# Optimization experiments

Measured on AMD Instinct MI355X. Metric: run time of the kernel, lower is better.

Reference implementation:

```python
import jax, jax.numpy as jnp
import numpy as np

B, L, H = 16, 32, 768
E, R, T = 200000, 512, 2000000
NUM_STEPS = 2
EPS = 1e-6


def setup_inputs() -> dict:
    key = jax.random.key(0)
    ks = jax.random.split(key, 16)
    s = 1.0 / np.sqrt(H)
    return {
        'heads': jax.random.uniform(ks[0], (B, E), jnp.float32),
        'q_word_h': jax.random.normal(ks[1], (B, L, H), jnp.float32),
        'attention_mask': jnp.ones((B, L), jnp.float32),
        'subj': jax.random.randint(ks[2], (T,), 0, E),
        'rel': jax.random.randint(ks[3], (T,), 0, R),
        'obj': jax.random.randint(ks[4], (T,), 0, E),
        'key_w': jax.random.normal(ks[5], (H, H), jnp.float32) * s,
        'key_b': jnp.zeros((H,), jnp.float32),
        'rel_w': jax.random.normal(ks[6], (H, R), jnp.float32) * s,
        'rel_b': jnp.zeros((R,), jnp.float32),
        'hop_w': jax.random.normal(ks[7], (H, 1), jnp.float32) * s,
        'hop_b': jnp.zeros((1,), jnp.float32),
        'hw_w': jax.random.normal(ks[8], (H, H), jnp.float32) * s,
        'hw_b': jnp.zeros((H,), jnp.float32),
    }


def _follow(e, r, subj, rel, obj, num_ent):
    # x[b,t] = e[b, subj[t]] * r[b, rel[t]]  (== Msubj@e.T * Mrel@r.T)
    x = e[:, subj] * r[:, rel]                      # [B, T]
    # scatter-add over object entities (== Mobj.T @ x)
    return jnp.zeros((e.shape[0], num_ent), e.dtype).at[:, obj].add(x)


def reference(heads, q_word_h, attention_mask, subj, rel, obj,
              key_w, key_b, rel_w, rel_b, hop_w, hop_b, hw_w, hw_b):
    mask = attention_mask[:, None, :]               # [B,1,L]
    last_e = heads
    q_hop = q_word_h
    prev_ctx = None                                  # q_word_h_dist_ctx[-1]
    ent_probs, ctx_h_list = [], []
    for t in range(NUM_STEPS):
        h_key = q_hop @ key_w + key_b                # [B,L,H]
        # torch: (h_key @ q_word_h^T)^T -> logits[b,i,j] = q_word_h[b,i].h_key[b,j]
        q_logits = jnp.einsum('bih,bjh->bij', q_word_h, h_key)
        q_dist = jax.nn.softmax(q_logits, axis=2) * mask
        q_dist = q_dist / (jnp.sum(q_dist, axis=2, keepdims=True) + EPS)
        hop_ctx = jnp.einsum('bij,bjh->bih', q_dist, q_hop)
        if t == 0:
            q_hop = q_word_h + hop_ctx
            prev_ctx = hop_ctx
        else:
            z = jax.nn.sigmoid(prev_ctx @ hw_w + hw_b)
            q_hop = q_word_h + hop_ctx + z * prev_ctx
            prev_ctx = hop_ctx + z * prev_ctx
        q_word_att = jax.nn.softmax(jnp.sum(q_dist, axis=1, keepdims=True), axis=2) * mask
        q_word_att = q_word_att / (jnp.sum(q_word_att, axis=2, keepdims=True) + EPS)  # [B,1,L]
        ctx_h = jnp.einsum('blh,bl->bh', q_hop, q_word_att[:, 0, :])
        ctx_h_list.append(ctx_h)
        rel_dist = jax.nn.sigmoid(ctx_h @ rel_w + rel_b)   # [B,R]
        new_e = _follow(last_e, rel_dist, subj, rel, obj, heads.shape[1])
        # clamp-by-division with detached scale
        z_norm = jax.lax.stop_gradient(jnp.where(new_e > 1.0, new_e, 1.0))
        last_e = new_e / z_norm
        ent_probs.append(last_e)
    hop_res = jnp.stack(ent_probs, axis=1)           # [B,S,E]
    ctx_hist = jnp.stack(ctx_h_list, axis=1)         # [B,S,H]
    hop_logit = ctx_hist @ hop_w + hop_b             # [B,S,1]
    hop_attn = jax.nn.softmax(hop_logit, axis=1)     # softmax over hops
    e_score = jnp.sum(hop_res * hop_attn, axis=1)    # [B,E]
    return e_score
```

## Files before the change

### kernel.cpp

```cpp
#include <hip/hip_runtime.h>
#include <hip/hip_bf16.h>
#include <math.h>

#define NB 16
#define NL 32
#define NH 768
#define NE 200000
#define NR 512
#define NT 2000000
#define FEPS 1e-6f

#define EB_BLOCKS ((NE + 255) / 256)

typedef float f32x4 __attribute__((ext_vector_type(4)));

__global__ __launch_bounds__(256) void k_transpose_zero(const float* __restrict__ heads,
                                                        float* __restrict__ headsT,
                                                        float* __restrict__ e0T,
                                                        float* __restrict__ e1T) {
  __shared__ float tile[256][17];
  int e0 = blockIdx.x * 256;
  int tid = threadIdx.x;
  if (e0 + tid < NE) {
#pragma unroll
    for (int b = 0; b < NB; ++b)
      tile[tid][b] = heads[(size_t)b * NE + e0 + tid];
  }
  {
    f32x4 z = {0.f, 0.f, 0.f, 0.f};
#pragma unroll
    for (int j = 0; j < 4; ++j) {
      int idx4 = j * 256 + tid;
      size_t base = (size_t)e0 * NB + idx4 * 4;
      if (base < (size_t)NE * NB) {
        *(f32x4*)(e0T + base) = z;
        *(f32x4*)(e1T + base) = z;
      }
    }
  }
  __syncthreads();
#pragma unroll
  for (int j = 0; j < 16; ++j) {
    int idx = j * 256 + tid;
    int i = idx >> 4, b = idx & 15;
    if (e0 + i < NE) headsT[(size_t)(e0 + i) * NB + b] = tile[i][b];
  }
}

__global__ __launch_bounds__(256) void k_rowmm2(const float* __restrict__ X0,
                                                const float* __restrict__ W0,
                                                const float* __restrict__ b0,
                                                float* __restrict__ Y0, int act0,
                                                const float* __restrict__ X1,
                                                const float* __restrict__ W1,
                                                const float* __restrict__ b1,
                                                float* __restrict__ Y1, int act1,
                                                int nblk0) {
  const float* X; const float* W; const float* bias; float* Y; int act, row0;
  int blk = blockIdx.x;
  if (blk < nblk0) { X = X0; W = W0; bias = b0; Y = Y0; act = act0; row0 = blk * 2; }
  else            { X = X1; W = W1; bias = b1; Y = Y1; act = act1; row0 = (blk - nblk0) * 2; }

  __shared__ float xs[2][NH];
  int tid = threadIdx.x;
  for (int r = 0; r < 2; ++r)
    for (int k = tid; k < NH; k += 256)
      xs[r][k] = X[(size_t)(row0 + r) * NH + k];
  __syncthreads();

  float acc[2][3] = {};
  for (int k = 0; k < NH; ++k) {
    float w0 = W[(size_t)k * NH + tid];
    float w1 = W[(size_t)k * NH + tid + 256];
    float w2 = W[(size_t)k * NH + tid + 512];
#pragma unroll
    for (int r = 0; r < 2; ++r) {
      float x = xs[r][k];
      acc[r][0] = fmaf(x, w0, acc[r][0]);
      acc[r][1] = fmaf(x, w1, acc[r][1]);
      acc[r][2] = fmaf(x, w2, acc[r][2]);
    }
  }
  float bb0 = bias[tid], bb1 = bias[tid + 256], bb2 = bias[tid + 512];
#pragma unroll
  for (int r = 0; r < 2; ++r) {
    size_t base = (size_t)(row0 + r) * NH;
    float y0 = acc[r][0] + bb0, y1 = acc[r][1] + bb1, y2 = acc[r][2] + bb2;
    if (act == 1) {
      y0 = 1.f / (1.f + expf(-y0));
      y1 = 1.f / (1.f + expf(-y1));
      y2 = 1.f / (1.f + expf(-y2));
    }
    Y[base + tid] = y0;
    Y[base + tid + 256] = y1;
    Y[base + tid + 512] = y2;
  }
}

template <int STEP>
__global__ __launch_bounds__(1024) void k_attn_update(const float* __restrict__ qwh,
                                                      const float* __restrict__ hkey,
                                                      const float* __restrict__ mask,
                                                      const float* __restrict__ qhop_old,
                                                      const float* __restrict__ zbuf,
                                                      const float* __restrict__ pc_old,
                                                      float* __restrict__ qhop_new,
                                                      float* __restrict__ pc_new,
                                                      float* __restrict__ ctx_h,
                                                      const float* __restrict__ rel_w,
                                                      const float* __restrict__ rel_b,
                                                      float* __restrict__ relT) {
  int b = blockIdx.x;
  int tid = threadIdx.x;
  __shared__ float qs_full[NL * NH];
  __shared__ float hks[32 * 129];
  __shared__ float qd[32 * 33];
  __shared__ float ctx_s[NH];
  __shared__ float as[NL];

#pragma unroll
  for (int it = 0; it < 6; ++it) {
    int idx4 = it * 1024 + tid;
    f32x4 v = *(const f32x4*)(qwh + (size_t)b * NL * NH + idx4 * 4);
    *(f32x4*)(qs_full + idx4 * 4) = v;
  }
  __syncthreads();

  int i = tid >> 5, j = tid & 31;
  float acc = 0.f;
  for (int k0 = 0; k0 < NH; k0 += 128) {
    {
      int jj = tid >> 5;
      int kk4 = tid & 31;
      f32x4 hv = *(const f32x4*)(hkey + ((size_t)b * NL + jj) * NH + k0 + kk4 * 4);
      int base = jj * 129 + kk4 * 4;
      hks[base] = hv.x; hks[base + 1] = hv.y; hks[base + 2] = hv.z; hks[base + 3] = hv.w;
    }
    __syncthreads();
#pragma unroll 8
    for (int kk = 0; kk < 128; ++kk)
      acc = fmaf(qs_full[i * NH + k0 + kk], hks[j * 129 + kk], acc);
    __syncthreads();
  }

  float m = acc;
  for (int s = 16; s; s >>= 1) m = fmaxf(m, __shfl_xor(m, s, 32));
  float ex = expf(acc - m);
  float sum = ex;
  for (int s = 16; s; s >>= 1) sum += __shfl_xor(sum, s, 32);
  float p = ex / sum;
  p *= mask[b * NL + j];
  float s2 = p;
  for (int s = 16; s; s >>= 1) s2 += __shfl_xor(s2, s, 32);
  p = p / (s2 + FEPS);
  qd[i * 33 + j] = p;
  __syncthreads();

  if (tid < 32) {
    int jj = tid;
    float c = 0.f;
    for (int ii = 0; ii < 32; ++ii) c += qd[ii * 33 + jj];
    float mm = c;
    for (int s = 16; s; s >>= 1) mm = fmaxf(mm, __shfl_xor(mm, s, 32));
    float e2 = expf(c - mm);
    float ss = e2;
    for (int s = 16; s; s >>= 1) ss += __shfl_xor(ss, s, 32);
    float a = e2 / ss;
    a *= mask[b * NL + jj];
    float s3 = a;
    for (int s = 16; s; s >>= 1) s3 += __shfl_xor(s3, s, 32);
    as[jj] = a / (s3 + FEPS);
  }
  __syncthreads();

  if (tid < NH) {
    int h = tid;
    float qh[NL];
#pragma unroll
    for (int jj = 0; jj < NL; ++jj) {
      if (STEP == 0)
        qh[jj] = qs_full[jj * NH + h];
      else
        qh[jj] = qhop_old[((size_t)b * NL + jj) * NH + h];
    }
    float c = 0.f;
    for (int l = 0; l < NL; ++l) {
      float hop = 0.f;
#pragma unroll
      for (int jj = 0; jj < NL; ++jj)
        hop = fmaf(qd[l * 33 + jj], qh[jj], hop);
      size_t base = ((size_t)b * NL + l) * NH + h;
      float qn;
      if (STEP == 0) {
        qn = qs_full[l * NH + h] + hop;
        qhop_new[base] = qn;
        pc_new[base] = hop;
      } else {
        float t = zbuf[base] * pc_old[base];
        qn = qs_full[l * NH + h] + hop + t;
      }
      c = fmaf(as[l], qn, c);
    }
    ctx_h[((size_t)b * 2 + STEP) * NH + h] = c;
    ctx_s[h] = c;
  }
  __syncthreads();

  if (tid < NR) {
    int r = tid;
    float a = rel_b[r];
    for (int h = 0; h < NH; ++h)
      a = fmaf(ctx_s[h], rel_w[(size_t)h * NR + r], a);
    relT[r * NB + b] = 1.f / (1.f + expf(-a));
  }
}

template <int CLAMP>
__global__ __launch_bounds__(256) void k_follow(const int* __restrict__ subj,
                                                const int* __restrict__ rel,
                                                const int* __restrict__ obj,
                                                const float* __restrict__ srcT,
                                                const float* __restrict__ relT,
                                                float* __restrict__ dstT) {
  const size_t stride = (size_t)gridDim.x * 256;
  size_t gid = (size_t)blockIdx.x * 256 + threadIdx.x;
#pragma unroll 4
  for (int it = 0; it < 4; ++it, gid += stride) {
    int k = (int)(gid >> 4);
    int b = (int)(gid & 15);
    int s = __builtin_nontemporal_load(&subj[k]);
    int r = __builtin_nontemporal_load(&rel[k]);
    int o = __builtin_nontemporal_load(&obj[k]);
    float x = srcT[(size_t)s * NB + b];
    if (CLAMP) x = fminf(x, 1.f);
    x *= relT[r * NB + b];
    atomicAdd(&dstT[(size_t)o * NB + b], x);
  }
}

__global__ __launch_bounds__(256) void k_combine(const float* __restrict__ e0T,
                                                 const float* __restrict__ e1T,
                                                 const float* __restrict__ ctx_h,
                                                 const float* __restrict__ hop_w,
                                                 const float* __restrict__ hop_b,
                                                 float* __restrict__ out) {
  __shared__ float s0[256 * 17], s1[256 * 17];
  __shared__ float lg[32];
  __shared__ float ha[32];
  int tid = threadIdx.x;

  {
    int pair = tid >> 3, sub = tid & 7;
    int bb = pair >> 1, t = pair & 1;
    float acc = 0.f;
    for (int h = sub; h < NH; h += 8)
      acc = fmaf(ctx_h[((size_t)bb * 2 + t) * NH + h], hop_w[h], acc);
    for (int s = 4; s; s >>= 1) acc += __shfl_xor(acc, s, 8);
    if (sub == 0) lg[pair] = acc + hop_b[0];
  }
  __syncthreads();
  if (tid < 16) {
    float l0 = lg[tid * 2], l1 = lg[tid * 2 + 1];
    float m = fmaxf(l0, l1);
    float e0 = expf(l0 - m), e1 = expf(l1 - m);
    float s = e0 + e1;
    ha[tid * 2] = e0 / s;
    ha[tid * 2 + 1] = e1 / s;
  }
  __syncthreads();

  int e0 = blockIdx.x * 256;
#pragma unroll
  for (int j = 0; j < 16; ++j) {
    int idx = j * 256 + tid;
    int i = idx >> 4, b = idx & 15;
    if (e0 + i < NE) {
      s0[i * 17 + b] = fminf(e0T[(size_t)e0 * NB + idx], 1.f);
      s1[i * 17 + b] = fminf(e1T[(size_t)e0 * NB + idx], 1.f);
    }
  }
  __syncthreads();
  if (e0 + tid < NE) {
#pragma unroll
    for (int b = 0; b < NB; ++b) {
      float a0 = ha[b * 2], a1 = ha[b * 2 + 1];
      out[(size_t)b * NE + e0 + tid] = a0 * s0[tid * 17 + b] + a1 * s1[tid * 17 + b];
    }
  }
}

extern "C" void kernel_launch(void* const* d_in, const int* in_sizes, int n_in,
                              void* d_out, int out_size, void* d_ws, size_t ws_size,
                              hipStream_t stream) {
  const float* heads = (const float*)d_in[0];
  const float* q_word_h = (const float*)d_in[1];
  const float* mask = (const float*)d_in[2];
  const int* subj = (const int*)d_in[3];
  const int* rel = (const int*)d_in[4];
  const int* obj = (const int*)d_in[5];
  const float* key_w = (const float*)d_in[6];
  const float* key_b = (const float*)d_in[7];
  const float* rel_w = (const float*)d_in[8];
  const float* rel_b = (const float*)d_in[9];
  const float* hop_w = (const float*)d_in[10];
  const float* hop_b = (const float*)d_in[11];
  const float* hw_w = (const float*)d_in[12];
  const float* hw_b = (const float*)d_in[13];

  float* ws = (float*)d_ws;
  size_t o = 0;
  float* headsT = ws + o; o += (size_t)NE * NB;
  float* e0T    = ws + o; o += (size_t)NE * NB;
  float* e1T    = ws + o; o += (size_t)NE * NB;
  float* h_key  = ws + o; o += (size_t)NB * NL * NH;
  float* qhopB  = ws + o; o += (size_t)NB * NL * NH;
  float* pcB    = ws + o; o += (size_t)NB * NL * NH;
  float* zbuf   = ws + o; o += (size_t)NB * NL * NH;
  float* ctx_h  = ws + o; o += (size_t)NB * 2 * NH;
  float* relT   = ws + o; o += (size_t)NR * NB;

  const int MM_BLOCKS = (NB * NL) / 2;
  const int FOLLOW_BLOCKS = (NT * 16) / (256 * 4);

  k_transpose_zero<<<EB_BLOCKS, 256, 0, stream>>>(heads, headsT, e0T, e1T);

  k_rowmm2<<<MM_BLOCKS, 256, 0, stream>>>(q_word_h, key_w, key_b, h_key, 0,
                                          q_word_h, key_w, key_b, h_key, 0, MM_BLOCKS);
  k_attn_update<0><<<NB, 1024, 0, stream>>>(q_word_h, h_key, mask, q_word_h,
                                            nullptr, nullptr, qhopB, pcB, ctx_h,
                                            rel_w, rel_b, relT);
  k_follow<0><<<FOLLOW_BLOCKS, 256, 0, stream>>>(subj, rel, obj, headsT, relT, e0T);

  k_rowmm2<<<2 * MM_BLOCKS, 256, 0, stream>>>(qhopB, key_w, key_b, h_key, 0,
                                              pcB, hw_w, hw_b, zbuf, 1, MM_BLOCKS);
  k_attn_update<1><<<NB, 1024, 0, stream>>>(q_word_h, h_key, mask, qhopB,
                                            zbuf, pcB, nullptr, nullptr, ctx_h,
                                            rel_w, rel_b, relT);
  k_follow<1><<<FOLLOW_BLOCKS, 256, 0, stream>>>(subj, rel, obj, e0T, relT, e1T);

  k_combine<<<EB_BLOCKS, 256, 0, stream>>>(e0T, e1T, ctx_h, hop_w, hop_b, (float*)d_out);
}
```

Baseline: 559.9 us.

## Merge independent kernels to overlap transpose with matmul and follow with matmul

Fuses the heads transpose/zeroing with the first key projection into a single launch using block-index dispatch. It also runs the step-1 matmuls (key projection and highway gate) in the same grid as the step-0 follow scatter, since those pieces are independent. The aim is to cut launch count and let small under-occupied matmul blocks run alongside the memory-bound gather/scatter work. The cost is more complex kernels with a shared smem footprint and mixed block types that may hurt scheduling.

```diff
diff --git a/kernel.cpp b/kernel.cpp
--- a/kernel.cpp
+++ b/kernel.cpp
@@ -11,61 +11,19 @@
 #define FEPS 1e-6f
 
 #define EB_BLOCKS ((NE + 255) / 256)
+#define FOLLOW_BLOCKS 31250
 
 typedef float f32x4 __attribute__((ext_vector_type(4)));
 
-__global__ __launch_bounds__(256) void k_transpose_zero(const float* __restrict__ heads,
-                                                        float* __restrict__ headsT,
-                                                        float* __restrict__ e0T,
-                                                        float* __restrict__ e1T) {
-  __shared__ float tile[256][17];
-  int e0 = blockIdx.x * 256;
-  int tid = threadIdx.x;
-  if (e0 + tid < NE) {
-#pragma unroll
-    for (int b = 0; b < NB; ++b)
-      tile[tid][b] = heads[(size_t)b * NE + e0 + tid];
-  }
-  {
-    f32x4 z = {0.f, 0.f, 0.f, 0.f};
-#pragma unroll
-    for (int j = 0; j < 4; ++j) {
-      int idx4 = j * 256 + tid;
-      size_t base = (size_t)e0 * NB + idx4 * 4;
-      if (base < (size_t)NE * NB) {
-        *(f32x4*)(e0T + base) = z;
-        *(f32x4*)(e1T + base) = z;
-      }
-    }
-  }
-  __syncthreads();
-#pragma unroll
-  for (int j = 0; j < 16; ++j) {
-    int idx = j * 256 + tid;
-    int i = idx >> 4, b = idx & 15;
-    if (e0 + i < NE) headsT[(size_t)(e0 + i) * NB + b] = tile[i][b];
-  }
-}
-
-__global__ __launch_bounds__(256) void k_rowmm2(const float* __restrict__ X0,
-                                                const float* __restrict__ W0,
-                                                const float* __restrict__ b0,
-                                                float* __restrict__ Y0, int act0,
-                                                const float* __restrict__ X1,
-                                                const float* __restrict__ W1,
-                                                const float* __restrict__ b1,
-                                                float* __restrict__ Y1, int act1,
-                                                int nblk0) {
-  const float* X; const float* W; const float* bias; float* Y; int act, row0;
-  int blk = blockIdx.x;
-  if (blk < nblk0) { X = X0; W = W0; bias = b0; Y = Y0; act = act0; row0 = blk * 2; }
-  else            { X = X1; W = W1; bias = b1; Y = Y1; act = act1; row0 = (blk - nblk0) * 2; }
-
-  __shared__ float xs[2][NH];
+__device__ __forceinline__ void rowmm_body(const float* __restrict__ X,
+                                           const float* __restrict__ W,
+                                           const float* __restrict__ bias,
+                                           float* __restrict__ Y, int act, int row0,
+                                           float* __restrict__ xs ) {
   int tid = threadIdx.x;
   for (int r = 0; r < 2; ++r)
     for (int k = tid; k < NH; k += 256)
-      xs[r][k] = X[(size_t)(row0 + r) * NH + k];
+      xs[r * NH + k] = X[(size_t)(row0 + r) * NH + k];
   __syncthreads();
 
   float acc[2][3] = {};
@@ -75,7 +33,7 @@
     float w2 = W[(size_t)k * NH + tid + 512];
 #pragma unroll
     for (int r = 0; r < 2; ++r) {
-      float x = xs[r][k];
+      float x = xs[r * NH + k];
       acc[r][0] = fmaf(x, w0, acc[r][0]);
       acc[r][1] = fmaf(x, w1, acc[r][1]);
       acc[r][2] = fmaf(x, w2, acc[r][2]);
@@ -94,6 +52,49 @@
     Y[base + tid] = y0;
     Y[base + tid + 256] = y1;
     Y[base + tid + 512] = y2;
+  }
+}
+
+__global__ __launch_bounds__(256) void k_pre(const float* __restrict__ heads,
+                                             float* __restrict__ headsT,
+                                             float* __restrict__ e0T,
+                                             float* __restrict__ e1T,
+                                             const float* __restrict__ qwh,
+                                             const float* __restrict__ key_w,
+                                             const float* __restrict__ key_b,
+                                             float* __restrict__ h_key) {
+  __shared__ float sm[256 * 17];
+  int blk = blockIdx.x;
+  int tid = threadIdx.x;
+  if (blk < EB_BLOCKS) {
+    float (*tile)[17] = (float (*)[17])sm;
+    int e0 = blk * 256;
+    if (e0 + tid < NE) {
+#pragma unroll
+      for (int b = 0; b < NB; ++b)
+        tile[tid][b] = heads[(size_t)b * NE + e0 + tid];
+    }
+    {
+      f32x4 z = {0.f, 0.f, 0.f, 0.f};
+#pragma unroll
+      for (int j = 0; j < 4; ++j) {
+        int idx4 = j * 256 + tid;
+        size_t base = (size_t)e0 * NB + idx4 * 4;
+        if (base < (size_t)NE * NB) {
+          *(f32x4*)(e0T + base) = z;
+          *(f32x4*)(e1T + base) = z;
+        }
+      }
+    }
+    __syncthreads();
+#pragma unroll
+    for (int j = 0; j < 16; ++j) {
+      int idx = j * 256 + tid;
+      int i = idx >> 4, b = idx & 15;
+      if (e0 + i < NE) headsT[(size_t)(e0 + i) * NB + b] = tile[i][b];
+    }
+  } else {
+    rowmm_body(qwh, key_w, key_b, h_key, 0, (blk - EB_BLOCKS) * 2, sm);
   }
 }
 
@@ -215,6 +216,45 @@
   }
 }
 
+__global__ __launch_bounds__(256) void k_follow_mm(const float* __restrict__ qhopB,
+                                                   const float* __restrict__ key_w,
+                                                   const float* __restrict__ key_b,
+                                                   float* __restrict__ h_key,
+                                                   const float* __restrict__ pcB,
+                                                   const float* __restrict__ hw_w,
+                                                   const float* __restrict__ hw_b,
+                                                   float* __restrict__ zbuf,
+                                                   const int* __restrict__ subj,
+                                                   const int* __restrict__ rel,
+                                                   const int* __restrict__ obj,
+                                                   const float* __restrict__ headsT,
+                                                   const float* __restrict__ relT,
+                                                   float* __restrict__ e0T) {
+  __shared__ float xs[2 * NH];
+  int blk = blockIdx.x;
+  if (blk < 256) {
+    rowmm_body(qhopB, key_w, key_b, h_key, 0, blk * 2, xs);
+    return;
+  }
+  if (blk < 512) {
+    rowmm_body(pcB, hw_w, hw_b, zbuf, 1, (blk - 256) * 2, xs);
+    return;
+  }
+  const size_t stride = (size_t)FOLLOW_BLOCKS * 256;
+  size_t gid = (size_t)(blk - 512) * 256 + threadIdx.x;
+#pragma unroll 4
+  for (int it = 0; it < 4; ++it, gid += stride) {
+    int k = (int)(gid >> 4);
+    int b = (int)(gid & 15);
+    int s = __builtin_nontemporal_load(&subj[k]);
+    int r = __builtin_nontemporal_load(&rel[k]);
+    int o = __builtin_nontemporal_load(&obj[k]);
+    float x = headsT[(size_t)s * NB + b];
+    x *= relT[r * NB + b];
+    atomicAdd(&e0T[(size_t)o * NB + b], x);
+  }
+}
+
 template <int CLAMP>
 __global__ __launch_bounds__(256) void k_follow(const int* __restrict__ subj,
                                                 const int* __restrict__ rel,
@@ -319,23 +359,22 @@
   float* ctx_h  = ws + o; o += (size_t)NB * 2 * NH;
   float* relT   = ws + o; o += (size_t)NR * NB;
 
-  const int MM_BLOCKS = (NB * NL) / 2;
-  const int FOLLOW_BLOCKS = (NT * 16) / (256 * 4);
-
-  k_transpose_zero<<<EB_BLOCKS, 256, 0, stream>>>(heads, headsT, e0T, e1T);
-
-  k_rowmm2<<<MM_BLOCKS, 256, 0, stream>>>(q_word_h, key_w, key_b, h_key, 0,
-                                          q_word_h, key_w, key_b, h_key, 0, MM_BLOCKS);
+  k_pre<<<EB_BLOCKS + 256, 256, 0, stream>>>(heads, headsT, e0T, e1T,
+                                             q_word_h, key_w, key_b, h_key);
+
   k_attn_update<0><<<NB, 1024, 0, stream>>>(q_word_h, h_key, mask, q_word_h,
                                             nullptr, nullptr, qhopB, pcB, ctx_h,
                                             rel_w, rel_b, relT);
-  k_follow<0><<<FOLLOW_BLOCKS, 256, 0, stream>>>(subj, rel, obj, headsT, relT, e0T);
-
-  k_rowmm2<<<2 * MM_BLOCKS, 256, 0, stream>>>(qhopB, key_w, key_b, h_key, 0,
-                                              pcB, hw_w, hw_b, zbuf, 1, MM_BLOCKS);
+
+  k_follow_mm<<<512 + FOLLOW_BLOCKS, 256, 0, stream>>>(qhopB, key_w, key_b, h_key,
+                                                       pcB, hw_w, hw_b, zbuf,
+                                                       subj, rel, obj,
+                                                       headsT, relT, e0T);
+
   k_attn_update<1><<<NB, 1024, 0, stream>>>(q_word_h, h_key, mask, qhopB,
                                             zbuf, pcB, nullptr, nullptr, ctx_h,
                                             rel_w, rel_b, relT);
+
   k_follow<1><<<FOLLOW_BLOCKS, 256, 0, stream>>>(subj, rel, obj, e0T, relT, e1T);
 
   k_combine<<<EB_BLOCKS, 256, 0, stream>>>(e0T, e1T, ctx_h, hop_w, hop_b, (float*)d_out);
```

Result: faster. 547.3 us (-2.3%).
